# Optimization experiments

Hardware: AMD Instinct MI355X
Metric: run time of the kernel (lower is better)

The kernel has to match this reference:

```python
import jax, jax.numpy as jnp
import numpy as np

N = 100000      # nodes
E = 3200000     # edges (avg degree 32)
F_IN = 512
F_OUT = 256


def setup_inputs() -> dict:
    key = jax.random.key(0)
    k1, k2, k3, k4, k5, k6 = jax.random.split(key, 6)
    x = jax.random.normal(k1, (N, F_IN), dtype=jnp.float32)
    row = jax.random.randint(k2, (E,), 0, N)            # destination node of each edge
    col = jax.random.randint(k3, (E,), 0, N)            # source node of each edge
    edge_val = jax.random.uniform(k4, (E,), dtype=jnp.float32)  # normalized adj weights
    stdv = 1.0 / np.sqrt(F_OUT)                         # matches reset_parameters()
    weight = jax.random.uniform(k5, (F_IN, F_OUT), dtype=jnp.float32, minval=-stdv, maxval=stdv)
    bias = jax.random.uniform(k6, (F_OUT,), dtype=jnp.float32, minval=-stdv, maxval=stdv)
    return {"input": x, "weight": weight, "bias": bias, "edge_val": edge_val, "row": row, "col": col}


def reference(input, weight, bias, edge_val, row, col):
    # support = X @ W  (dense projection)
    support = input @ weight                             # [N, F_OUT]
    # SpMM: out[r] += a[r,c] * support[c] over COO edges (torch.spmm(adj, support))
    msgs = edge_val[:, None] * support[col]              # [E, F_OUT] gather + scale
    agg = jax.ops.segment_sum(msgs, row, num_segments=input.shape[0])  # scatter-add
    # np.around(..., decimals=3) applied row-wise in the original
    out = jnp.round(agg * 1000.0) / 1000.0
    return out + bias
```

## Files before the change

### kernel.cpp

```cpp
#include <hip/hip_runtime.h>
#include <hip/hip_bf16.h>

#define N_NODES 100000
#define N_EDGES 3200000
#define FIN 512
#define FOUT 256
#define GEMM_BM 128
#define GEMM_BK 32

#define NP 782
#define CAP_LDS 4608
#define SC_CHUNK 16384

typedef __attribute__((ext_vector_type(8))) short short8;
typedef __attribute__((ext_vector_type(4))) float f32x4;

__device__ __forceinline__ unsigned short f2bf(float f) {
    unsigned u = __float_as_uint(f);
    u += 0x7fffu + ((u >> 16) & 1u);
    return (unsigned short)(u >> 16);
}
__device__ __forceinline__ float bf2f(unsigned short h) {
    return __uint_as_float(((unsigned)h) << 16);
}

__device__ __forceinline__ void gload_lds16(const void* g, void* l) {
    __builtin_amdgcn_global_load_lds(
        (const __attribute__((address_space(1))) unsigned*)g,
        (__attribute__((address_space(3))) unsigned*)l, 16, 0, 0);
}

__global__ __launch_bounds__(256) void prep_weight(const float* __restrict__ W,
                                                   unsigned short* __restrict__ Wt) {
    int idx = blockIdx.x * 256 + threadIdx.x;
    if (idx < FIN * FOUT) {
        int k = idx >> 8;
        int n = idx & 255;
        int s = k >> 5;
        int kk = k & 31;
        int kb16 = kk >> 3;
        int u = kb16 ^ (n & 3) ^ ((n >> 2) & 3);
        Wt[(size_t)s * 8192 + n * 32 + u * 8 + (kk & 7)] = f2bf(W[idx]);
    }
}

__global__ __launch_bounds__(512, 2)
void gemm_kernel(const float* __restrict__ X, const unsigned short* __restrict__ Wt,
                 unsigned short* __restrict__ support) {
    __shared__ unsigned short A_lds[GEMM_BM][40];
    __shared__ __align__(16) unsigned short bls[8192];

    const int t = threadIdx.x;
    const int lane = t & 63;
    const int w = t >> 6;
    const int wm = w >> 2;
    const int wn = w & 3;
    const int q = lane >> 4;
    const int lr = lane & 15;
    const int m0 = blockIdx.x * GEMM_BM;

    f32x4 acc[4][4];
#pragma unroll
    for (int i = 0; i < 4; i++)
#pragma unroll
        for (int j = 0; j < 4; j++) acc[i][j] = (f32x4)0.0f;

    const int arow = t >> 2;
    const int acol = (t & 3) * 8;
    const bool avalid = (m0 + arow) < N_NODES;
    const float* Xp = X + (size_t)(m0 + arow) * FIN + acol;

    const unsigned short* gB = Wt + t * 8;
    unsigned short* ldsB0 = &bls[w * 512];
    unsigned short* ldsB1 = &bls[4096 + w * 512];

    for (int s = 0; s < FIN / GEMM_BK; ++s) {
        union { __hip_bfloat162 h[4]; uint4 v; } pk;
        if (avalid) {
            float4 v0 = *(const float4*)(Xp + s * GEMM_BK);
            float4 v1 = *(const float4*)(Xp + s * GEMM_BK + 4);
            pk.h[0] = __float22bfloat162_rn(make_float2(v0.x, v0.y));
            pk.h[1] = __float22bfloat162_rn(make_float2(v0.z, v0.w));
            pk.h[2] = __float22bfloat162_rn(make_float2(v1.x, v1.y));
            pk.h[3] = __float22bfloat162_rn(make_float2(v1.z, v1.w));
        } else {
            pk.v = make_uint4(0, 0, 0, 0);
        }

        __syncthreads();

        gload_lds16(gB + (size_t)s * 8192, ldsB0);
        gload_lds16(gB + (size_t)s * 8192 + 4096, ldsB1);

        *(uint4*)&A_lds[arow][acol] = pk.v;

        __syncthreads();

        short8 af[4], bfr[4];
#pragma unroll
        for (int i = 0; i < 4; i++) af[i] = *(const short8*)&A_lds[wm * 64 + i * 16 + lr][q * 8];
#pragma unroll
        for (int j = 0; j < 4; j++) {
            int nl = wn * 64 + j * 16 + lr;
            int u = q ^ (nl & 3) ^ ((nl >> 2) & 3);
            bfr[j] = *(const short8*)&bls[nl * 32 + u * 8];
        }
#pragma unroll
        for (int i = 0; i < 4; i++)
#pragma unroll
            for (int j = 0; j < 4; j++)
                acc[i][j] = __builtin_amdgcn_mfma_f32_16x16x32_bf16(af[i], bfr[j], acc[i][j], 0, 0, 0);
    }

#pragma unroll
    for (int i = 0; i < 4; i++) {
#pragma unroll
        for (int r = 0; r < 4; r++) {
            int gm = m0 + wm * 64 + i * 16 + q * 4 + r;
            if (gm < N_NODES) {
#pragma unroll
                for (int j = 0; j < 4; j++)
                    support[(size_t)gm * FOUT + wn * 64 + j * 16 + lr] = f2bf(acc[i][j][r]);
            }
        }
    }
}

__global__ __launch_bounds__(256) void part_hist(const int* __restrict__ row,
                                                 unsigned* __restrict__ pcnt) {
    __shared__ unsigned bins[NP];
    for (int i = threadIdx.x; i < NP; i += 256) bins[i] = 0;
    __syncthreads();
    const int e0 = blockIdx.x * 8192;
#pragma unroll
    for (int j = 0; j < 32; ++j) {
        int e = e0 + j * 256 + threadIdx.x;
        if (e < N_EDGES) atomicAdd(&bins[((unsigned)row[e]) >> 7], 1u);
    }
    __syncthreads();
    for (int i = threadIdx.x; i < NP; i += 256)
        if (bins[i]) atomicAdd(&pcnt[i], bins[i]);
}

__global__ __launch_bounds__(1024) void part_scan(const unsigned* __restrict__ pcnt,
                                                  unsigned* __restrict__ base,
                                                  unsigned* __restrict__ cursor,
                                                  unsigned* __restrict__ row_ptr) {
    __shared__ unsigned s[1024];
    const int t = threadIdx.x;
    unsigned v = (t < NP) ? pcnt[t] : 0u;
    s[t] = v;
    __syncthreads();
#pragma unroll
    for (int off = 1; off < 1024; off <<= 1) {
        unsigned tv = (t >= off) ? s[t - off] : 0u;
        __syncthreads();
        s[t] += tv;
        __syncthreads();
    }
    if (t < NP) {
        unsigned b = s[t] - v;
        base[t] = b;
        cursor[t] = b;
    }
    if (t == 0) {
        base[NP] = N_EDGES;
        row_ptr[N_NODES] = N_EDGES;
    }
}

__global__ __launch_bounds__(256) void part_scatter(const int* __restrict__ row,
                                                    const int* __restrict__ col,
                                                    const float* __restrict__ val,
                                                    unsigned* __restrict__ cursor,
                                                    uint2* __restrict__ part) {
    __shared__ unsigned bins[NP];
    __shared__ unsigned gb[NP];
    for (int i = threadIdx.x; i < NP; i += 256) bins[i] = 0;
    __syncthreads();
    const int e0 = blockIdx.x * SC_CHUNK;
#pragma unroll 4
    for (int j = 0; j < SC_CHUNK / 256; ++j) {
        int e = e0 + j * 256 + threadIdx.x;
        if (e < N_EDGES) atomicAdd(&bins[((unsigned)row[e]) >> 7], 1u);
    }
    __syncthreads();
    for (int i = threadIdx.x; i < NP; i += 256) {
        unsigned c = bins[i];
        gb[i] = c ? atomicAdd(&cursor[i], c) : 0u;
        bins[i] = 0;
    }
    __syncthreads();
#pragma unroll 4
    for (int j = 0; j < SC_CHUNK / 256; ++j) {
        int e = e0 + j * 256 + threadIdx.x;
        if (e < N_EDGES) {
            unsigned r = (unsigned)row[e];
            unsigned p = r >> 7;
            unsigned l = atomicAdd(&bins[p], 1u);
            part[gb[p] + l] = make_uint2(((unsigned)col[e]) | ((r & 127u) << 17),
                                         __float_as_uint(val[e]));
        }
    }
}

__global__ __launch_bounds__(256) void part_finalize(const unsigned* __restrict__ base,
                                                     uint2* __restrict__ part,
                                                     unsigned* __restrict__ row_ptr) {
    __shared__ uint2 recs[CAP_LDS];
    __shared__ unsigned ncnt[128], nsc[128], ccur[128];
    const int p = blockIdx.x;
    const int t = threadIdx.x;
    const unsigned b = base[p];
    unsigned cnt = base[p + 1] - b;
    if (cnt > CAP_LDS) cnt = CAP_LDS;
    if (t < 128) ncnt[t] = 0;
    __syncthreads();
    for (unsigned i = t; i < cnt; i += 256) {
        uint2 r = part[b + i];
        recs[i] = r;
        atomicAdd(&ncnt[r.x >> 17], 1u);
    }
    __syncthreads();
    if (t < 128) nsc[t] = ncnt[t];
    __syncthreads();
#pragma unroll
    for (int off = 1; off < 128; off <<= 1) {
        unsigned tv = (t < 128 && t >= off) ? nsc[t - off] : 0u;
        __syncthreads();
        if (t < 128) nsc[t] += tv;
        __syncthreads();
    }
    if (t < 128) {
        unsigned ex = nsc[t] - ncnt[t];
        ccur[t] = ex;
        int node = p * 128 + t;
        if (node < N_NODES) row_ptr[node] = b + ex;
    }
    __syncthreads();
    for (unsigned i = t; i < cnt; i += 256) {
        uint2 r = recs[i];
        unsigned pos = atomicAdd(&ccur[r.x >> 17], 1u);
        part[b + pos] = make_uint2(r.x & 0x1FFFFu, r.y);
    }
}

__global__ __launch_bounds__(256)
void spmm_kernel(const unsigned* __restrict__ row_ptr, const uint2* __restrict__ sorted,
                 const unsigned short* __restrict__ support, const float* __restrict__ bias,
                 float* __restrict__ out) {
    const int lane = threadIdx.x & 63;
    const int n = blockIdx.x * 4 + (threadIdx.x >> 6);
    const unsigned start = __builtin_amdgcn_readfirstlane(row_ptr[n]);
    const unsigned end   = __builtin_amdgcn_readfirstlane(row_ptr[n + 1]);
    const int fo = (blockIdx.y << 7) + lane * 2;
    const unsigned short* sp = support + fo;
    float a0 = 0.f, a1 = 0.f;

    unsigned i = start;
    const unsigned nfull = (end - start) >> 4;
    if (nfull) {
        uint2 e[16];
#pragma unroll
        for (int j = 0; j < 16; ++j) e[j] = sorted[i + j];
        for (unsigned bt = 1; bt < nfull; ++bt) {
            ushort2 s[16];
#pragma unroll
            for (int j = 0; j < 16; ++j) s[j] = *(const ushort2*)(sp + (size_t)e[j].x * FOUT);
            uint2 en[16];
#pragma unroll
            for (int j = 0; j < 16; ++j) en[j] = sorted[i + 16 + j];
#pragma unroll
            for (int j = 0; j < 16; ++j) {
                float v = __uint_as_float(e[j].y);
                a0 += v * bf2f(s[j].x); a1 += v * bf2f(s[j].y);
            }
#pragma unroll
            for (int j = 0; j < 16; ++j) e[j] = en[j];
            i += 16;
        }
        ushort2 s[16];
#pragma unroll
        for (int j = 0; j < 16; ++j) s[j] = *(const ushort2*)(sp + (size_t)e[j].x * FOUT);
#pragma unroll
        for (int j = 0; j < 16; ++j) {
            float v = __uint_as_float(e[j].y);
            a0 += v * bf2f(s[j].x); a1 += v * bf2f(s[j].y);
        }
        i += 16;
    }
    if (end - i >= 8) {
        uint2 e[8];
#pragma unroll
        for (int j = 0; j < 8; ++j) e[j] = sorted[i + j];
        ushort2 s[8];
#pragma unroll
        for (int j = 0; j < 8; ++j) s[j] = *(const ushort2*)(sp + (size_t)e[j].x * FOUT);
#pragma unroll
        for (int j = 0; j < 8; ++j) {
            float v = __uint_as_float(e[j].y);
            a0 += v * bf2f(s[j].x); a1 += v * bf2f(s[j].y);
        }
        i += 8;
    }
    for (; i < end; ++i) {
        uint2 e = sorted[i];
        float v = __uint_as_float(e.y);
        ushort2 s0 = *(const ushort2*)(sp + (size_t)e.x * FOUT);
        a0 += v * bf2f(s0.x); a1 += v * bf2f(s0.y);
    }

    float2 bv = *(const float2*)(bias + fo);
    float2 r;
    r.x = rintf(a0 * 1000.f) * 0.001f + bv.x;
    r.y = rintf(a1 * 1000.f) * 0.001f + bv.y;
    *(float2*)(out + (size_t)n * FOUT + fo) = r;
}

extern "C" void kernel_launch(void* const* d_in, const int* in_sizes, int n_in,
                              void* d_out, int out_size, void* d_ws, size_t ws_size,
                              hipStream_t stream) {
    (void)in_sizes; (void)n_in; (void)out_size; (void)ws_size;
    const float* X    = (const float*)d_in[0];
    const float* W    = (const float*)d_in[1];
    const float* bias = (const float*)d_in[2];
    const float* eval = (const float*)d_in[3];
    const int*   row  = (const int*)d_in[4];
    const int*   col  = (const int*)d_in[5];
    float* out = (float*)d_out;

    char* p = (char*)d_ws;
    auto take = [&](size_t bytes) {
        char* r = p;
        p += (bytes + 511) & ~(size_t)511;
        return r;
    };
    unsigned short* support = (unsigned short*)take((size_t)N_NODES * FOUT * 2);
    unsigned short* Wt      = (unsigned short*)take((size_t)FIN * FOUT * 2);
    unsigned*       pcnt    = (unsigned*)take((size_t)NP * 4);
    unsigned*       base    = (unsigned*)take((size_t)(NP + 1) * 4);
    unsigned*       cursor  = (unsigned*)take((size_t)NP * 4);
    unsigned*       row_ptr = (unsigned*)take((size_t)(N_NODES + 1) * 4);
    uint2*          part    = (uint2*)take((size_t)N_EDGES * 8 + 1024);

    hipMemsetAsync(pcnt, 0, (size_t)NP * 4, stream);
    prep_weight<<<(FIN * FOUT) / 256, 256, 0, stream>>>(W, Wt);
    gemm_kernel<<<(N_NODES + GEMM_BM - 1) / GEMM_BM, 512, 0, stream>>>(X, Wt, support);
    part_hist<<<(N_EDGES + 8191) / 8192, 256, 0, stream>>>(row, pcnt);
    part_scan<<<1, 1024, 0, stream>>>(pcnt, base, cursor, row_ptr);
    part_scatter<<<(N_EDGES + SC_CHUNK - 1) / SC_CHUNK, 256, 0, stream>>>(row, col, eval, cursor, part);
    part_finalize<<<NP, 256, 0, stream>>>(base, part, row_ptr);
    spmm_kernel<<<dim3(N_NODES / 4, 2), 256, 0, stream>>>(row_ptr, part, support, bias, out);
}
```

Baseline: 705.0 us.

## Widen edge partitions to 256 rows and split SpMM into per-half launches

Doubles the row-partition size used for COO-to-CSR sorting, halving the number of partitions and finalize blocks while enlarging the LDS staging buffer. The SpMM is launched twice sequentially, once per 128-feature half, instead of as one 2D grid. The intent is to cut partition overhead and improve cache locality of gathered support rows per launch. It adds more LDS use per finalize block and an extra kernel launch.

```diff
diff --git a/kernel.cpp b/kernel.cpp
--- a/kernel.cpp
+++ b/kernel.cpp
@@ -8,8 +8,10 @@
 #define GEMM_BM 128
 #define GEMM_BK 32
 
-#define NP 782
-#define CAP_LDS 4608
+#define PSZ 256
+#define PSH 8
+#define NP 391
+#define CAP_LDS 8960
 #define SC_CHUNK 16384
 
 typedef __attribute__((ext_vector_type(8))) short short8;
@@ -135,7 +137,7 @@
 #pragma unroll
     for (int j = 0; j < 32; ++j) {
         int e = e0 + j * 256 + threadIdx.x;
-        if (e < N_EDGES) atomicAdd(&bins[((unsigned)row[e]) >> 7], 1u);
+        if (e < N_EDGES) atomicAdd(&bins[((unsigned)row[e]) >> PSH], 1u);
     }
     __syncthreads();
     for (int i = threadIdx.x; i < NP; i += 256)
@@ -182,7 +184,7 @@
 #pragma unroll 4
     for (int j = 0; j < SC_CHUNK / 256; ++j) {
         int e = e0 + j * 256 + threadIdx.x;
-        if (e < N_EDGES) atomicAdd(&bins[((unsigned)row[e]) >> 7], 1u);
+        if (e < N_EDGES) atomicAdd(&bins[((unsigned)row[e]) >> PSH], 1u);
     }
     __syncthreads();
     for (int i = threadIdx.x; i < NP; i += 256) {
@@ -196,9 +198,9 @@
         int e = e0 + j * 256 + threadIdx.x;
         if (e < N_EDGES) {
             unsigned r = (unsigned)row[e];
-            unsigned p = r >> 7;
+            unsigned p = r >> PSH;
             unsigned l = atomicAdd(&bins[p], 1u);
-            part[gb[p] + l] = make_uint2(((unsigned)col[e]) | ((r & 127u) << 17),
+            part[gb[p] + l] = make_uint2(((unsigned)col[e]) | ((r & (PSZ - 1u)) << 17),
                                          __float_as_uint(val[e]));
         }
     }
@@ -208,13 +210,13 @@
                                                      uint2* __restrict__ part,
                                                      unsigned* __restrict__ row_ptr) {
     __shared__ uint2 recs[CAP_LDS];
-    __shared__ unsigned ncnt[128], nsc[128], ccur[128];
+    __shared__ unsigned ncnt[PSZ], nsc[PSZ], ccur[PSZ];
     const int p = blockIdx.x;
     const int t = threadIdx.x;
     const unsigned b = base[p];
     unsigned cnt = base[p + 1] - b;
     if (cnt > CAP_LDS) cnt = CAP_LDS;
-    if (t < 128) ncnt[t] = 0;
+    ncnt[t] = 0;
     __syncthreads();
     for (unsigned i = t; i < cnt; i += 256) {
         uint2 r = part[b + i];
@@ -222,19 +224,19 @@
         atomicAdd(&ncnt[r.x >> 17], 1u);
     }
     __syncthreads();
-    if (t < 128) nsc[t] = ncnt[t];
-    __syncthreads();
-#pragma unroll
-    for (int off = 1; off < 128; off <<= 1) {
-        unsigned tv = (t < 128 && t >= off) ? nsc[t - off] : 0u;
-        __syncthreads();
-        if (t < 128) nsc[t] += tv;
-        __syncthreads();
-    }
-    if (t < 128) {
+    nsc[t] = ncnt[t];
+    __syncthreads();
+#pragma unroll
+    for (int off = 1; off < PSZ; off <<= 1) {
+        unsigned tv = (t >= off) ? nsc[t - off] : 0u;
+        __syncthreads();
+        nsc[t] += tv;
+        __syncthreads();
+    }
+    {
         unsigned ex = nsc[t] - ncnt[t];
         ccur[t] = ex;
-        int node = p * 128 + t;
+        int node = p * PSZ + t;
         if (node < N_NODES) row_ptr[node] = b + ex;
     }
     __syncthreads();
@@ -248,12 +250,12 @@
 __global__ __launch_bounds__(256)
 void spmm_kernel(const unsigned* __restrict__ row_ptr, const uint2* __restrict__ sorted,
                  const unsigned short* __restrict__ support, const float* __restrict__ bias,
-                 float* __restrict__ out) {
+                 float* __restrict__ out, int fb) {
     const int lane = threadIdx.x & 63;
     const int n = blockIdx.x * 4 + (threadIdx.x >> 6);
     const unsigned start = __builtin_amdgcn_readfirstlane(row_ptr[n]);
     const unsigned end   = __builtin_amdgcn_readfirstlane(row_ptr[n + 1]);
-    const int fo = (blockIdx.y << 7) + lane * 2;
+    const int fo = fb + lane * 2;
     const unsigned short* sp = support + fo;
     float a0 = 0.f, a1 = 0.f;
 
@@ -350,5 +352,6 @@
     part_scan<<<1, 1024, 0, stream>>>(pcnt, base, cursor, row_ptr);
     part_scatter<<<(N_EDGES + SC_CHUNK - 1) / SC_CHUNK, 256, 0, stream>>>(row, col, eval, cursor, part);
     part_finalize<<<NP, 256, 0, stream>>>(base, part, row_ptr);
-    spmm_kernel<<<dim3(N_NODES / 4, 2), 256, 0, stream>>>(row_ptr, part, support, bias, out);
-}
+    spmm_kernel<<<N_NODES / 4, 256, 0, stream>>>(row_ptr, part, support, bias, out, 0);
+    spmm_kernel<<<N_NODES / 4, 256, 0, stream>>>(row_ptr, part, support, bias, out, 128);
+}
```

New measurement: 702.6 us. No clear change (-0.3%).
